# Kernel optimization log

Hardware: AMD Instinct MI355X
Metric: run time of the kernel (lower is better)

## Reference

```python
import jax, jax.numpy as jnp
import numpy as np
from jax import lax

B, G, D, S = 1, 2048, 64, 2
H_FULL = 200
H0 = H_FULL // 2 ** (S - 1)
PC_RANGE = (-50.0, -50.0, -4.0, 50.0, 50.0, 4.0)
THRESH = 0.05
CHUNK = 128


def conv3x3(x, w):
    # x: [b,c,h,w], w: [o,i,3,3]
    return lax.conv_general_dilated(x, w, (1, 1), 'SAME',
                                    dimension_numbers=('NCHW', 'OIHW', 'NCHW'))


def instance_norm(x, eps=1e-5):
    mu = x.mean(axis=(2, 3), keepdims=True)
    var = x.var(axis=(2, 3), keepdims=True)
    return (x - mu) / jnp.sqrt(var + eps)


def basic_block(x, w1, w2):
    # conv-(BN@init=identity)-relu-conv-(BN)-add-relu
    h = jax.nn.relu(conv3x3(x, w1))
    h = conv3x3(h, w2)
    return jax.nn.relu(x + h)


def upsampling_add(x, skip, w):
    b, c, h, wd = x.shape
    xu = jax.image.resize(x, (b, c, 2 * h, 2 * wd), method='bilinear')
    xu = instance_norm(conv3x3(xu, w))
    return xu + skip


def render_stage(means, cov6, feats, opac, mask, H, W):
    # Orthographic BEV splatting (3DGS-style EWA + front-to-back compositing).
    g, d = feats.shape
    sh = H / 100.0
    sw = W / 100.0
    # full_proj_transform: px = -sh*y + H/2 ; py = -sw*x + W/2
    u = -sh * means[:, 1] + 0.5 * H
    v = -sw * means[:, 0] + 0.5 * W
    # cov2d = J Sigma J^T + 0.3*I, J = [[0,-sh,0],[-sw,0,0]]
    a = sh * sh * cov6[:, 3] + 0.3
    c = sw * sw * cov6[:, 0] + 0.3
    bb = sh * sw * cov6[:, 1]
    det = jnp.maximum(a * c - bb * bb, 1e-8)
    A = c / det
    Bc = -bb / det
    C = a / det
    xs = jnp.arange(W, dtype=jnp.float32)
    ys = jnp.arange(H, dtype=jnp.float32)
    nc = g // CHUNK

    def step(carry, inp):
        T, out = carry
        u_, v_, A_, B_, C_, op_, mk_, ft_ = inp
        dx = u_[:, None, None] - xs[None, None, :]
        dy = v_[:, None, None] - ys[None, :, None]
        power = (-0.5 * (A_[:, None, None] * dx * dx + C_[:, None, None] * dy * dy)
                 - B_[:, None, None] * dx * dy)
        alpha = jnp.minimum(op_[:, None, None] * jnp.exp(power), 0.99)
        alpha = jnp.where((alpha >= 1.0 / 255.0) & mk_[:, None, None] & (power <= 0.0),
                          alpha, 0.0)
        cp = jnp.cumprod(1.0 - alpha, axis=0)
        t_exc = jnp.concatenate([jnp.ones_like(cp[:1]), cp[:-1]], 0) * T
        out = out + jnp.einsum('ghw,gd->dhw', alpha * t_exc, ft_)
        return (T * cp[-1], out), None

    ch = lambda arr: arr.reshape(nc, CHUNK, *arr.shape[1:])
    init = (jnp.ones((H, W), jnp.float32), jnp.zeros((d, H, W), jnp.float32))
    (_, out), _ = lax.scan(step, init,
                           (ch(u), ch(v), ch(A), ch(Bc), ch(C), ch(opac), ch(mask), ch(feats)))
    return out  # bg color = 0


def setup_inputs() -> dict:
    key = jax.random.key(0)
    ks = jax.random.split(key, 10)
    features = jax.random.normal(ks[0], (B, G, D), jnp.float32)
    xy = jax.random.uniform(ks[1], (B, G, 2), jnp.float32, -55.0, 55.0)
    z = jax.random.uniform(ks[2], (B, G, 1), jnp.float32, -5.0, 5.0)
    means3D = jnp.concatenate([xy, z], -1)
    L = jax.random.normal(ks[3], (B, G, 3, 3), jnp.float32) * 0.5
    Sig = jnp.einsum('bgij,bgkj->bgik', L, L) + 0.1 * jnp.eye(3, dtype=jnp.float32)
    cov3D = jnp.stack([Sig[..., 0, 0], Sig[..., 0, 1], Sig[..., 0, 2],
                       Sig[..., 1, 1], Sig[..., 1, 2], Sig[..., 2, 2]], -1)
    opacities = jax.random.uniform(ks[4], (B, G, S), jnp.float32)
    w_scale = 1.0 / np.sqrt(D * 9)
    bev_emb = jax.random.normal(ks[5], (H0 * H0, D), jnp.float32) * 0.02
    conv1_w = jax.random.normal(ks[6], (S, D, D, 3, 3), jnp.float32) * w_scale
    blk_w = jax.random.normal(ks[7], (S, 2, 2, D, D, 3, 3), jnp.float32) * w_scale
    up_w = jax.random.normal(ks[8], (S - 1, D, D, 3, 3), jnp.float32) * w_scale
    return {'features': features, 'means3D': means3D, 'cov3D': cov3D,
            'opacities': opacities, 'bev_emb': bev_emb, 'conv1_w': conv1_w,
            'blk_w': blk_w, 'up_w': up_w}


def reference(features, means3D, cov3D, opacities, bev_emb, conv1_w, blk_w, up_w):
    b = features.shape[0]
    d = features.shape[-1]
    m = means3D
    mask_pos = ((m[..., 0] >= PC_RANGE[0]) & (m[..., 0] <= PC_RANGE[3]) &
                (m[..., 1] >= PC_RANGE[1]) & (m[..., 1] <= PC_RANGE[4]) &
                (m[..., 2] >= PC_RANGE[2]) & (m[..., 2] <= PC_RANGE[5]))
    num_g = jnp.float32(0.0)
    bevs = []
    for s in range(S):
        H = H0 * 2 ** s
        mask = (opacities[..., s] > THRESH) & mask_pos
        rend = jax.vmap(lambda mn, cv, ft, op, mk: render_stage(mn, cv, ft, op, mk, H, H))
        bevs.append(rend(means3D, cov3D, features, opacities[..., s], mask))
        num_g = num_g + jnp.mean(jnp.sum(mask.astype(jnp.float32), 1))
    x = jnp.broadcast_to(jnp.transpose(bev_emb.reshape(H0, H0, d), (2, 0, 1))[None],
                         (b, d, H0, H0))
    for s in range(S):
        bev = conv3x3(bevs[s], conv1_w[s])
        if s == 0:
            x = x + bev
        else:
            x = upsampling_add(x, bev, up_w[s - 1])
        for blk in range(2):
            x = basic_block(x, blk_w[s, blk, 0], blk_w[s, blk, 1])
    return x, num_g
```

## Files before the change

### kernel.cpp

```cpp
#include <hip/hip_runtime.h>
#include <math.h>

#define G_N 2048
#define CCH 256
#define PSTR 12
#define NBLK 1024
#define WC (64 * 64 * 9)

typedef short bhalf8 __attribute__((ext_vector_type(8)));
typedef float f32x4 __attribute__((ext_vector_type(4)));
typedef unsigned short u16;

__device__ __forceinline__ u16 f2bf(float f) {
    unsigned u = __float_as_uint(f);
    unsigned r = (u + 0x7fffu + ((u >> 16) & 1u)) >> 16;
    return (u16)r;
}
__device__ __forceinline__ float b2f(u16 h) {
    return __uint_as_float((unsigned)h << 16);
}

__device__ __forceinline__ void chstore4(u16* p, ushort4 v) {
    union { unsigned long long u; ushort4 s; } x; x.s = v;
    __hip_atomic_store((unsigned long long*)p, x.u,
                       __ATOMIC_RELAXED, __HIP_MEMORY_SCOPE_AGENT);
}
__device__ __forceinline__ void cstore8(float* p, float a, float b) {
    union { unsigned long long u; float f[2]; } x;
    x.f[0] = a; x.f[1] = b;
    __hip_atomic_store((unsigned long long*)p, x.u,
                       __ATOMIC_RELAXED, __HIP_MEMORY_SCOPE_AGENT);
}
__device__ __forceinline__ float cload(const float* p) {
    return __hip_atomic_load(p, __ATOMIC_RELAXED, __HIP_MEMORY_SCOPE_AGENT);
}
__device__ __forceinline__ int iload(const int* p) {
    return __hip_atomic_load(p, __ATOMIC_RELAXED, __HIP_MEMORY_SCOPE_AGENT);
}

__device__ __forceinline__ void gbar(int* leaf, int* root, int* flag, int phase) {
    asm volatile("s_waitcnt vmcnt(0) lgkmcnt(0)" ::: "memory");
    __syncthreads();
    if (threadIdx.x == 0) {
        int g = blockIdx.x >> 5;
        int old = atomicAdd(&leaf[g * 16], 1);
        if ((old & 31) == 31) {
            int o2 = atomicAdd(root, 1);
            if ((o2 & 31) == 31)
                __hip_atomic_store(flag, phase, __ATOMIC_RELAXED,
                                   __HIP_MEMORY_SCOPE_AGENT);
        }
        while (__hip_atomic_load(flag, __ATOMIC_RELAXED,
                                 __HIP_MEMORY_SCOPE_AGENT) < phase)
            __builtin_amdgcn_s_sleep(16);
    }
    __syncthreads();
    asm volatile("" ::: "memory");
}

__device__ __forceinline__ void render_tile(
    int unit, const float* __restrict__ params,
    const float* __restrict__ feats, u16* __restrict__ out0,
    u16* __restrict__ out1, char* smem)
{
    int s = (unit < 169) ? 0 : 1;
    int t = (s == 0) ? unit : unit - 169;
    int tw = (s == 0) ? 13 : 25;
    int bxx = t % tw, byy = t / tw;
    int H = 100 << s;
    const float* P = params + s * G_N * PSTR;
    u16* out = s ? out1 : out0;

    float* raw = (float*)smem;
    float* cmp = raw + CCH * PSTR;
    int* s_wsum = (int*)(smem + 24576);

    int tid = threadIdx.x;
    int w = tid >> 6, lane = tid & 63;
    int x0 = bxx * 8, y0 = byy * 8;
    int px = x0 + (lane & 7), py = y0 + (lane >> 3);
    bool active = (px < H) && (py < H);
    float fx = (float)px, fy = (float)py;
    float tx0 = (float)x0, tx1 = (float)min(H - 1, x0 + 7);
    float ty0 = (float)y0, ty1 = (float)min(H - 1, y0 + 7);

    f32x4 acc[4];
#pragma unroll
    for (int k = 0; k < 4; ++k) acc[k] = (f32x4){0.f, 0.f, 0.f, 0.f};
    float T = 1.f;

    for (int base = 0; base < G_N; base += CCH) {
        int anyalive = __syncthreads_or((int)(active && T > 1e-6f));
        if (!anyalive) break;
        for (int i = tid; i < CCH * 3; i += 256)
            ((float4*)raw)[i] = ((const float4*)(P + base * PSTR))[i];
        __syncthreads();
        float u = raw[tid * PSTR + 0], v = raw[tid * PSTR + 1];
        float rx = raw[tid * PSTR + 8], ry = raw[tid * PSTR + 9];
        bool pass = (u + rx >= tx0) && (u - rx <= tx1) &&
                    (v + ry >= ty0) && (v - ry <= ty1);
        unsigned long long bal = __ballot(pass);
        int prefix = __popcll(bal & ((1ull << lane) - 1ull));
        if (lane == 0) s_wsum[w] = __popcll(bal);
        __syncthreads();
        int woff = 0;
        for (int k = 0; k < 4; ++k) if (k < w) woff += s_wsum[k];
        if (pass) {
            float4* dst = (float4*)(cmp + (woff + prefix) * PSTR);
            const float4* src = (const float4*)(raw + tid * PSTR);
            dst[0] = src[0]; dst[1] = src[1]; dst[2] = src[2];
        }
        __syncthreads();
        int nc = s_wsum[0] + s_wsum[1] + s_wsum[2] + s_wsum[3];
        if (active && T > 1e-6f) {
            for (int j = 0; j < nc; ++j) {
                float4 q0 = *(const float4*)(cmp + j * PSTR);
                float4 q1 = *(const float4*)(cmp + j * PSTR + 4);
                float dx = q0.x - fx, dy = q0.y - fy;
                float power = -0.5f * (q0.z * dx * dx + q1.x * dy * dy) - q0.w * dx * dy;
                if (power <= 0.f && power >= q1.z) {
                    float alpha = fminf(q1.y * __expf(power), 0.99f);
                    float wgt = alpha * T;
                    const f32x4* f4 = (const f32x4*)(feats + __float_as_int(q1.w) * 64) + w * 4;
#pragma unroll
                    for (int k = 0; k < 4; ++k) {
                        f32x4 fv = f4[k];
                        acc[k][0] = fmaf(wgt, fv[0], acc[k][0]);
                        acc[k][1] = fmaf(wgt, fv[1], acc[k][1]);
                        acc[k][2] = fmaf(wgt, fv[2], acc[k][2]);
                        acc[k][3] = fmaf(wgt, fv[3], acc[k][3]);
                    }
                    T *= (1.f - alpha);
                }
            }
        }
    }

    __syncthreads();
    float* shf = (float*)smem;
#pragma unroll
    for (int k = 0; k < 4; ++k)
        *(float4*)&shf[lane * 68 + w * 16 + k * 4] =
            (float4){acc[k][0], acc[k][1], acc[k][2], acc[k][3]};
    __syncthreads();
    for (int j = tid; j < 1024; j += 256) {
        int lp = j >> 4, c4 = (j & 15) * 4;
        int gy = y0 + (lp >> 3), gx = x0 + (lp & 7);
        if (gy < H && gx < H) {
            float4 v = *(float4*)&shf[lp * 68 + c4];
            ushort4 o = { f2bf(v.x), f2bf(v.y), f2bf(v.z), f2bf(v.w) };
            chstore4(&out[((gy * H + gx) << 6) + c4], o);
        }
    }
}

__device__ __forceinline__ void conv_tile(
    int bx, int H, const u16* __restrict__ in, const u16* __restrict__ wp,
    const float* __restrict__ bev, u16* __restrict__ outb,
    int ups, int dostats, float* __restrict__ sacc, char* smem)
{
    u16* xlds = (u16*)smem;
    u16* fin  = (u16*)(smem + 14400);
    float* red = (float*)(smem + 25600);

    int tid = threadIdx.x;
    int gw = (H + 7) >> 3;
    int by = bx / gw, bxx = bx - by * gw;
    int y0 = by * 8, x0 = bxx * 8;
    int w = tid >> 6, lane = tid & 63;
    int n = lane & 15, q = lane >> 4;
    int Hh = H >> 1;
    int oy = (y0 >> 1) - 2, ox = (x0 >> 1) - 2;

    if (ups) {
        for (int i = tid; i < 512; i += 256) {
            int px = i >> 3, c8 = (i & 7) * 8;
            int iy = px >> 3, ix = px & 7;
            int gyi = oy + iy, gxi = ox + ix;
            uint4 v = {0, 0, 0, 0};
            if (gyi >= 0 && gyi < Hh && gxi >= 0 && gxi < Hh)
                v = *(const uint4*)&in[((gyi * Hh + gxi) << 6) + c8];
            *(uint4*)&fin[px * 72 + c8] = v;
        }
        __syncthreads();
        for (int i = tid; i < 1600; i += 256) {
            int px = i >> 4, c4 = (i & 15) * 4;
            int yy = px / 10, xx = px - yy * 10;
            int gy = y0 - 1 + yy, gx = x0 - 1 + xx;
            ushort4 v = {0, 0, 0, 0};
            if (gy >= 0 && gy < H && gx >= 0 && gx < H) {
                int yi = gy >> 1, xi = gx >> 1;
                int yb = (gy & 1) ? min(yi + 1, Hh - 1) : max(yi - 1, 0);
                int xb = (gx & 1) ? min(xi + 1, Hh - 1) : max(xi - 1, 0);
                int t0 = yi - oy, t1 = xi - ox, t2 = yb - oy, t3 = xb - ox;
                ushort4 f00 = *(const ushort4*)&fin[(t0 * 8 + t1) * 72 + c4];
                ushort4 f01 = *(const ushort4*)&fin[(t0 * 8 + t3) * 72 + c4];
                ushort4 f10 = *(const ushort4*)&fin[(t2 * 8 + t1) * 72 + c4];
                ushort4 f11 = *(const ushort4*)&fin[(t2 * 8 + t3) * 72 + c4];
                v.x = f2bf(0.5625f * b2f(f00.x) + 0.1875f * (b2f(f01.x) + b2f(f10.x)) + 0.0625f * b2f(f11.x));
                v.y = f2bf(0.5625f * b2f(f00.y) + 0.1875f * (b2f(f01.y) + b2f(f10.y)) + 0.0625f * b2f(f11.y));
                v.z = f2bf(0.5625f * b2f(f00.z) + 0.1875f * (b2f(f01.z) + b2f(f10.z)) + 0.0625f * b2f(f11.z));
                v.w = f2bf(0.5625f * b2f(f00.w) + 0.1875f * (b2f(f01.w) + b2f(f10.w)) + 0.0625f * b2f(f11.w));
            }
            *(ushort4*)&xlds[px * 72 + c4] = v;
        }
    } else {
        for (int i = tid; i < 800; i += 256) {
            int px = i >> 3, c8 = (i & 7) * 8;
            int yy = px / 10, xx = px - yy * 10;
            int gy = y0 - 1 + yy, gx = x0 - 1 + xx;
            uint4 v = {0, 0, 0, 0};
            if (gy >= 0 && gy < H && gx >= 0 && gx < H)
                v = *(const uint4*)&in[((gy * H + gx) << 6) + c8];
            *(uint4*)&xlds[px * 72 + c8] = v;
        }
    }
    __syncthreads();

    f32x4 acc[4];
#pragma unroll
    for (int m = 0; m < 4; ++m) acc[m] = (f32x4){0.f, 0.f, 0.f, 0.f};
    const bhalf8* wp8 = (const bhalf8*)wp;
    int sy = 2 * w + (n >> 3), sx = n & 7;

    bhalf8 a0 = wp8[0 * 64 + lane];
    bhalf8 a1 = wp8[1 * 64 + lane];
    bhalf8 a2 = wp8[2 * 64 + lane];
    bhalf8 a3 = wp8[3 * 64 + lane];
    bhalf8 bb = *(const bhalf8*)&xlds[(sy * 10 + sx) * 72 + q * 8];

#pragma unroll 1
    for (int p = 0; p < 18; ++p) {
        bhalf8 na0, na1, na2, na3, nbb;
        if (p < 17) {
            int pn = p + 1;
            na0 = wp8[(pn * 4 + 0) * 64 + lane];
            na1 = wp8[(pn * 4 + 1) * 64 + lane];
            na2 = wp8[(pn * 4 + 2) * 64 + lane];
            na3 = wp8[(pn * 4 + 3) * 64 + lane];
            int tap = pn >> 1, ch = pn & 1;
            int dy = tap / 3, dx = tap - dy * 3;
            nbb = *(const bhalf8*)&xlds[((sy + dy) * 10 + sx + dx) * 72 + ch * 32 + q * 8];
        }
        acc[0] = __builtin_amdgcn_mfma_f32_16x16x32_bf16(a0, bb, acc[0], 0, 0, 0);
        acc[1] = __builtin_amdgcn_mfma_f32_16x16x32_bf16(a1, bb, acc[1], 0, 0, 0);
        acc[2] = __builtin_amdgcn_mfma_f32_16x16x32_bf16(a2, bb, acc[2], 0, 0, 0);
        acc[3] = __builtin_amdgcn_mfma_f32_16x16x32_bf16(a3, bb, acc[3], 0, 0, 0);
        a0 = na0; a1 = na1; a2 = na2; a3 = na3; bb = nbb;
    }

    int gy = y0 + sy, gx = x0 + sx;
    if (gy < H && gx < H) {
        int base = (gy * H + gx) << 6;
#pragma unroll
        for (int m = 0; m < 4; ++m) {
            int oc0 = m * 16 + q * 4;
            float v0 = acc[m][0], v1 = acc[m][1], v2 = acc[m][2], v3 = acc[m][3];
            if (bev) {
                float4 av = *(const float4*)&bev[base + oc0];
                v0 += av.x; v1 += av.y; v2 += av.z; v3 += av.w;
            }
            ushort4 o = { f2bf(v0), f2bf(v1), f2bf(v2), f2bf(v3) };
            chstore4(&outb[base + oc0], o);
        }
    }

    if (dostats) {
#pragma unroll
        for (int m = 0; m < 4; ++m)
#pragma unroll
            for (int r = 0; r < 4; ++r) {
                float v = acc[m][r];
                float s = v, s2 = v * v;
#pragma unroll
                for (int d = 1; d < 16; d <<= 1) {
                    s += __shfl_xor(s, d, 64);
                    s2 += __shfl_xor(s2, d, 64);
                }
                if (n == 0) {
                    int oc = m * 16 + q * 4 + r;
                    red[w * 128 + oc] = s;
                    red[w * 128 + 64 + oc] = s2;
                }
            }
        __syncthreads();
        if (tid < 128) {
            float t = red[tid] + red[128 + tid] + red[256 + tid] + red[384 + tid];
            atomicAdd(&sacc[tid], t);
        }
    }
}

__device__ __forceinline__ void bb_tile(
    int bx, int H, const u16* __restrict__ in,
    const u16* __restrict__ wp1, const u16* __restrict__ wp2,
    u16* __restrict__ outb, float* __restrict__ outf, int final_,
    int nrm, const u16* __restrict__ nskip, const float* __restrict__ sraw,
    char* smem)
{
    u16* xin  = (u16*)smem;
    u16* ilds = (u16*)(smem + 20736);
    float* nm = (float*)(smem + 35136);
    float* nr = nm + 64;

    int tid = threadIdx.x;
    int gw = (H + 7) >> 3;
    int by = bx / gw, bxx = bx - by * gw;
    int y0 = by * 8, x0 = bxx * 8;
    int w = tid >> 6, lane = tid & 63;
    int n = lane & 15, q = lane >> 4;

    if (nrm) {
        if (tid < 64) {
            float s = cload(&sraw[tid]), s2 = cload(&sraw[64 + tid]);
            float mean = s * (1.f / 40000.f);
            float var = s2 * (1.f / 40000.f) - mean * mean;
            nm[tid] = mean;
            nr[tid] = rsqrtf(var + 1e-5f);
        }
        __syncthreads();
        for (int i = tid; i < 2304; i += 256) {
            int px = i >> 4, c4 = (i & 15) * 4;
            int yy = px / 12, xx = px - yy * 12;
            int gy = y0 - 2 + yy, gx = x0 - 2 + xx;
            ushort4 v = {0, 0, 0, 0};
            if (gy >= 0 && gy < H && gx >= 0 && gx < H) {
                int off = ((gy * H + gx) << 6) + c4;
                ushort4 a = *(const ushort4*)&in[off];
                ushort4 b = *(const ushort4*)&nskip[off];
                v.x = f2bf((b2f(a.x) - nm[c4 + 0]) * nr[c4 + 0] + b2f(b.x));
                v.y = f2bf((b2f(a.y) - nm[c4 + 1]) * nr[c4 + 1] + b2f(b.y));
                v.z = f2bf((b2f(a.z) - nm[c4 + 2]) * nr[c4 + 2] + b2f(b.z));
                v.w = f2bf((b2f(a.w) - nm[c4 + 3]) * nr[c4 + 3] + b2f(b.w));
            }
            *(ushort4*)&xin[px * 72 + c4] = v;
        }
    } else {
        for (int i = tid; i < 1152; i += 256) {
            int px = i >> 3, c8 = (i & 7) * 8;
            int yy = px / 12, xx = px - yy * 12;
            int gy = y0 - 2 + yy, gx = x0 - 2 + xx;
            uint4 v = {0, 0, 0, 0};
            if (gy >= 0 && gy < H && gx >= 0 && gx < H)
                v = *(const uint4*)&in[((gy * H + gx) << 6) + c8];
            *(uint4*)&xin[px * 72 + c8] = v;
        }
    }
    __syncthreads();

    const bhalf8* w1 = (const bhalf8*)wp1;
#pragma unroll 1
    for (int r = 0; r < 2; ++r) {
        int t = w + 4 * r;
        int px = t * 16 + n;
        bool val = px < 100;
        int pc = val ? px : 0;
        int yy = pc / 10, xx = pc - yy * 10;

        f32x4 acc[4];
#pragma unroll
        for (int m = 0; m < 4; ++m) acc[m] = (f32x4){0.f, 0.f, 0.f, 0.f};

        bhalf8 a0 = w1[0 * 64 + lane];
        bhalf8 a1 = w1[1 * 64 + lane];
        bhalf8 a2 = w1[2 * 64 + lane];
        bhalf8 a3 = w1[3 * 64 + lane];
        bhalf8 bb = *(const bhalf8*)&xin[(yy * 12 + xx) * 72 + q * 8];

#pragma unroll 1
        for (int p = 0; p < 18; ++p) {
            bhalf8 na0, na1, na2, na3, nbb;
            if (p < 17) {
                int pn = p + 1;
                na0 = w1[(pn * 4 + 0) * 64 + lane];
                na1 = w1[(pn * 4 + 1) * 64 + lane];
                na2 = w1[(pn * 4 + 2) * 64 + lane];
                na3 = w1[(pn * 4 + 3) * 64 + lane];
                int tap = pn >> 1, ch = pn & 1;
                int dy = tap / 3, dx = tap - dy * 3;
                nbb = *(const bhalf8*)&xin[((yy + dy) * 12 + xx + dx) * 72 + ch * 32 + q * 8];
            }
            acc[0] = __builtin_amdgcn_mfma_f32_16x16x32_bf16(a0, bb, acc[0], 0, 0, 0);
            acc[1] = __builtin_amdgcn_mfma_f32_16x16x32_bf16(a1, bb, acc[1], 0, 0, 0);
            acc[2] = __builtin_amdgcn_mfma_f32_16x16x32_bf16(a2, bb, acc[2], 0, 0, 0);
            acc[3] = __builtin_amdgcn_mfma_f32_16x16x32_bf16(a3, bb, acc[3], 0, 0, 0);
            a0 = na0; a1 = na1; a2 = na2; a3 = na3; bb = nbb;
        }

        int iy = y0 - 1 + yy, ix = x0 - 1 + xx;
        bool ok = val && iy >= 0 && iy < H && ix >= 0 && ix < H;
        if (val) {
#pragma unroll
            for (int m = 0; m < 4; ++m) {
                ushort4 o = {0, 0, 0, 0};
                if (ok) {
                    o.x = f2bf(fmaxf(acc[m][0], 0.f));
                    o.y = f2bf(fmaxf(acc[m][1], 0.f));
                    o.z = f2bf(fmaxf(acc[m][2], 0.f));
                    o.w = f2bf(fmaxf(acc[m][3], 0.f));
                }
                *(ushort4*)&ilds[px * 72 + m * 16 + q * 4] = o;
            }
        }
    }
    __syncthreads();

    f32x4 acc[4];
#pragma unroll
    for (int m = 0; m < 4; ++m) acc[m] = (f32x4){0.f, 0.f, 0.f, 0.f};
    const bhalf8* w2 = (const bhalf8*)wp2;
    int sy = 2 * w + (n >> 3), sx = n & 7;

    bhalf8 a0 = w2[0 * 64 + lane];
    bhalf8 a1 = w2[1 * 64 + lane];
    bhalf8 a2 = w2[2 * 64 + lane];
    bhalf8 a3 = w2[3 * 64 + lane];
    bhalf8 bb = *(const bhalf8*)&ilds[(sy * 10 + sx) * 72 + q * 8];

#pragma unroll 1
    for (int p = 0; p < 18; ++p) {
        bhalf8 na0, na1, na2, na3, nbb;
        if (p < 17) {
            int pn = p + 1;
            na0 = w2[(pn * 4 + 0) * 64 + lane];
            na1 = w2[(pn * 4 + 1) * 64 + lane];
            na2 = w2[(pn * 4 + 2) * 64 + lane];
            na3 = w2[(pn * 4 + 3) * 64 + lane];
            int tap = pn >> 1, ch = pn & 1;
            int dy = tap / 3, dx = tap - dy * 3;
            nbb = *(const bhalf8*)&ilds[((sy + dy) * 10 + sx + dx) * 72 + ch * 32 + q * 8];
        }
        acc[0] = __builtin_amdgcn_mfma_f32_16x16x32_bf16(a0, bb, acc[0], 0, 0, 0);
        acc[1] = __builtin_amdgcn_mfma_f32_16x16x32_bf16(a1, bb, acc[1], 0, 0, 0);
        acc[2] = __builtin_amdgcn_mfma_f32_16x16x32_bf16(a2, bb, acc[2], 0, 0, 0);
        acc[3] = __builtin_amdgcn_mfma_f32_16x16x32_bf16(a3, bb, acc[3], 0, 0, 0);
        a0 = na0; a1 = na1; a2 = na2; a3 = na3; bb = nbb;
    }

    int gy = y0 + sy, gx = x0 + sx;
    if (gy < H && gx < H) {
        int base = (gy * H + gx) << 6;
#pragma unroll
        for (int m = 0; m < 4; ++m) {
            int oc0 = m * 16 + q * 4;
            ushort4 xr = *(const ushort4*)&xin[((sy + 2) * 12 + sx + 2) * 72 + oc0];
            float v0 = fmaxf(acc[m][0] + b2f(xr.x), 0.f);
            float v1 = fmaxf(acc[m][1] + b2f(xr.y), 0.f);
            float v2 = fmaxf(acc[m][2] + b2f(xr.z), 0.f);
            float v3 = fmaxf(acc[m][3] + b2f(xr.w), 0.f);
            if (final_) {
                int pix = gy * H + gx;
                outf[(oc0 + 0) * H * H + pix] = v0;
                outf[(oc0 + 1) * H * H + pix] = v1;
                outf[(oc0 + 2) * H * H + pix] = v2;
                outf[(oc0 + 3) * H * H + pix] = v3;
            } else {
                ushort4 o = { f2bf(v0), f2bf(v1), f2bf(v2), f2bf(v3) };
                chstore4(&outb[base + oc0], o);
            }
        }
    }
}

__global__ __launch_bounds__(256, 4) void gls_mega(
    const float* __restrict__ feats, const float* __restrict__ bev_emb,
    const float* __restrict__ conv1_w, const float* __restrict__ blk_w,
    const float* __restrict__ up_w, const float* __restrict__ means,
    const float* __restrict__ cov6, const float* __restrict__ opac,
    u16* __restrict__ wprep, float* __restrict__ params, int* __restrict__ cnts,
    u16* __restrict__ R0h, u16* __restrict__ X0h,
    u16* __restrict__ X1h, u16* __restrict__ X2h,
    u16* __restrict__ Qr0h, u16* __restrict__ Sh,
    u16* __restrict__ Uh, u16* __restrict__ Y1h,
    float* __restrict__ out, int* __restrict__ barmem, float* __restrict__ sacc)
{
    __shared__ __align__(16) char smem[36352];
    int bid = blockIdx.x;
    int tid = threadIdx.x;
    int* leaf = barmem;
    int* root = barmem + 512;
    int* flag = barmem + 513;
    int ph = 0;

    if (bid < 16) {
        int item = bid * 256 + tid;
        int s = item >> 11, g = item & 2047;
        float mx = means[g * 3 + 0], my = means[g * 3 + 1], mz = means[g * 3 + 2];
        float op = opac[g * 2 + s];
        bool mask = (mx >= -50.f && mx <= 50.f && my >= -50.f && my <= 50.f &&
                     mz >= -4.f && mz <= 4.f && op > 0.05f);
        float Hs = (float)(100 << s), sh = (float)(1 << s);
        float u = 0.f, v = 0.f, A = 0.f, B = 0.f, C = 0.f, pthr = 0.f;
        float rx = -1.f, ry = -1.f;
        if (mask) {
            u = -sh * my + 0.5f * Hs;
            v = -sh * mx + 0.5f * Hs;
            float a = sh * sh * cov6[g * 6 + 3] + 0.3f;
            float c = sh * sh * cov6[g * 6 + 0] + 0.3f;
            float bb = sh * sh * cov6[g * 6 + 1];
            float det = fmaxf(a * c - bb * bb, 1e-8f);
            float t = logf(255.f * op);
            A = c / det; B = -bb / det; C = a / det;
            pthr = -t;
            rx = sqrtf(2.f * t * a); ry = sqrtf(2.f * t * c);
        }
        float* Q = params + (s * G_N + g) * PSTR;
        cstore8(&Q[0], u, v);
        cstore8(&Q[2], A, B);
        cstore8(&Q[4], C, op);
        cstore8(&Q[6], pthr, __int_as_float(g));
        cstore8(&Q[8], rx, ry);
        unsigned long long bal = __ballot(mask);
        if ((tid & 63) == 0) atomicAdd(&cnts[s], __popcll(bal));
    }
    gbar(leaf, root, flag, ++ph);

    if (bid < 794) {
        render_tile(bid, params, feats, R0h, Qr0h, smem);
    } else if (bid < 992) {
        int rb = bid - 794;
        int p = rb % 18, c = rb / 18;
        const float* src;
        if (c == 0) src = conv1_w;
        else if (c <= 4) src = blk_w + (c - 1) * WC;
        else if (c == 5) src = conv1_w + WC;
        else if (c == 6) src = up_w;
        else src = blk_w + (c - 3) * WC;
        int tap = p >> 1;
        int m = tid >> 6, lane = tid & 63;
        int oc = m * 16 + (lane & 15);
        int ci0 = (p & 1) * 32 + (lane >> 4) * 8;
        u16 v[8];
#pragma unroll
        for (int j = 0; j < 8; ++j)
            v[j] = f2bf(src[(oc * 64 + ci0 + j) * 9 + tap]);
        u16* dst = wprep + ((c * 18 + p) * 4 + m) * 64 * 8 + lane * 8;
        chstore4(dst, (ushort4){v[0], v[1], v[2], v[3]});
        chstore4(dst + 4, (ushort4){v[4], v[5], v[6], v[7]});
    }
    gbar(leaf, root, flag, ++ph);

    if (bid < 169)
        conv_tile(bid, 100, R0h, wprep + 0 * WC, bev_emb, X0h, 0, 0, nullptr, smem);
    gbar(leaf, root, flag, ++ph);

    if (bid < 169)
        bb_tile(bid, 100, X0h, wprep + 1 * WC, wprep + 2 * WC, X1h,
                nullptr, 0, 0, nullptr, nullptr, smem);
    else if (bid < 481)
        conv_tile(bid - 169, 200, Qr0h, wprep + 5 * WC, nullptr, Sh, 0, 0, nullptr, smem);
    gbar(leaf, root, flag, ++ph);

    if (bid < 169)
        bb_tile(bid, 100, X1h, wprep + 3 * WC, wprep + 4 * WC, X2h,
                nullptr, 0, 0, nullptr, nullptr, smem);
    else if (bid < 482)
        conv_tile(312 + bid - 169, 200, Qr0h, wprep + 5 * WC, nullptr, Sh, 0, 0, nullptr, smem);
    gbar(leaf, root, flag, ++ph);

    if (bid < 625)
        conv_tile(bid, 200, X2h, wprep + 6 * WC, nullptr, Uh, 1, 1, sacc, smem);
    gbar(leaf, root, flag, ++ph);

    if (bid < 625)
        bb_tile(bid, 200, Uh, wprep + 7 * WC, wprep + 8 * WC, Y1h,
                nullptr, 0, 1, Sh, sacc, smem);
    gbar(leaf, root, flag, ++ph);

    if (bid == 0 && threadIdx.x == 0)
        out[2560000] = (float)(iload(&cnts[0]) + iload(&cnts[1]));
    if (bid < 625)
        bb_tile(bid, 200, Y1h, wprep + 9 * WC, wprep + 10 * WC, nullptr,
                out, 1, 0, nullptr, nullptr, smem);
}

extern "C" void kernel_launch(void* const* d_in, const int* in_sizes, int n_in,
                              void* d_out, int out_size, void* d_ws, size_t ws_size,
                              hipStream_t stream)
{
    const float* feats   = (const float*)d_in[0];
    const float* means   = (const float*)d_in[1];
    const float* cov6    = (const float*)d_in[2];
    const float* opac    = (const float*)d_in[3];
    const float* bev_emb = (const float*)d_in[4];
    const float* conv1_w = (const float*)d_in[5];
    const float* blk_w   = (const float*)d_in[6];
    const float* up_w    = (const float*)d_in[7];
    float* out = (float*)d_out;
    float* ws = (float*)d_ws;

    float* P      = ws;
    int*   cnts   = (int*)(ws + 49152);
    int*   barmem = (int*)(ws + 49280);
    float* sacc   = ws + 49856;
    u16*   wprep  = (u16*)(ws + 50176);

    u16* R0h  = (u16*)(ws + 262144);
    u16* X0h  = (u16*)(ws + 589824);
    u16* X1h  = (u16*)(ws + 917504);
    u16* X2h  = (u16*)(ws + 1245184);
    u16* Qr0h = (u16*)(ws + 1572864);
    u16* Sh   = (u16*)(ws + 2883584);
    u16* Uh   = (u16*)(ws + 4194304);
    u16* Y1h  = (u16*)(ws + 5505024);

    hipMemsetAsync(cnts, 0, (49984 - 49152) * 4, stream);
    gls_mega<<<NBLK, 256, 0, stream>>>(feats, bev_emb, conv1_w, blk_w, up_w,
                                       means, cov6, opac, wprep, P, cnts,
                                       R0h, X0h, X1h, X2h, Qr0h, Sh, Uh, Y1h,
                                       out, barmem, sacc);
    (void)in_sizes; (void)n_in; (void)out_size; (void)ws_size;
}
```

Baseline: 260.0 us.

## Triple-buffer MFMA operand prefetch and stage conv outputs through LDS for wide stores

Replaces the single-step software pipeline in the conv and basic-block MFMA loops with a fully unrolled loop that prefetches weights and LDS activations three steps ahead. This is meant to hide global/LDS load latency behind the MFMA chain. Conv and render epilogues now gather each tile's output in LDS and write 16-byte-per-thread contiguous stores instead of scattered 8-byte ones, at the cost of extra __syncthreads and higher register pressure under the 4-waves-per-SIMD launch bound.

```diff
diff --git a/kernel.cpp b/kernel.cpp
--- a/kernel.cpp
+++ b/kernel.cpp
@@ -20,16 +20,21 @@
     return __uint_as_float((unsigned)h << 16);
 }
 
-__device__ __forceinline__ void chstore4(u16* p, ushort4 v) {
-    union { unsigned long long u; ushort4 s; } x; x.s = v;
-    __hip_atomic_store((unsigned long long*)p, x.u,
+__device__ __forceinline__ void chstore8u(void* p, unsigned long long u) {
+    __hip_atomic_store((unsigned long long*)p, u,
                        __ATOMIC_RELAXED, __HIP_MEMORY_SCOPE_AGENT);
+}
+__device__ __forceinline__ void chstore16(void* p, uint4 v) {
+    union { uint2 d; unsigned long long u; } a, b;
+    a.d = (uint2){v.x, v.y};
+    b.d = (uint2){v.z, v.w};
+    chstore8u(p, a.u);
+    chstore8u((char*)p + 8, b.u);
 }
 __device__ __forceinline__ void cstore8(float* p, float a, float b) {
     union { unsigned long long u; float f[2]; } x;
     x.f[0] = a; x.f[1] = b;
-    __hip_atomic_store((unsigned long long*)p, x.u,
-                       __ATOMIC_RELAXED, __HIP_MEMORY_SCOPE_AGENT);
+    chstore8u(p, x.u);
 }
 __device__ __forceinline__ float cload(const float* p) {
     return __hip_atomic_load(p, __ATOMIC_RELAXED, __HIP_MEMORY_SCOPE_AGENT);
@@ -57,6 +62,40 @@
     __syncthreads();
     asm volatile("" ::: "memory");
 }
+
+#define KLOOP3(WPTR, LDSPTR, SY, SX, ACC)                                      \
+    {                                                                          \
+        const bhalf8* wp8_ = (const bhalf8*)(WPTR);                            \
+        bhalf8 A0_[3], A1_[3], A2_[3], A3_[3], Bv_[3];                         \
+        _Pragma("unroll")                                                      \
+        for (int i_ = 0; i_ < 3; ++i_) {                                       \
+            A0_[i_] = wp8_[(i_ * 4 + 0) * 64 + lane];                          \
+            A1_[i_] = wp8_[(i_ * 4 + 1) * 64 + lane];                          \
+            A2_[i_] = wp8_[(i_ * 4 + 2) * 64 + lane];                          \
+            A3_[i_] = wp8_[(i_ * 4 + 3) * 64 + lane];                          \
+            int tap_ = i_ >> 1, ch_ = i_ & 1;                                  \
+            int dy_ = tap_ / 3, dx_ = tap_ - dy_ * 3;                          \
+            Bv_[i_] = *(const bhalf8*)&(LDSPTR)[(((SY) + dy_) * 10 + (SX) + dx_) * 72 + ch_ * 32 + q * 8]; \
+        }                                                                      \
+        _Pragma("unroll")                                                      \
+        for (int p_ = 0; p_ < 18; ++p_) {                                      \
+            int sl_ = p_ % 3;                                                  \
+            ACC[0] = __builtin_amdgcn_mfma_f32_16x16x32_bf16(A0_[sl_], Bv_[sl_], ACC[0], 0, 0, 0); \
+            ACC[1] = __builtin_amdgcn_mfma_f32_16x16x32_bf16(A1_[sl_], Bv_[sl_], ACC[1], 0, 0, 0); \
+            ACC[2] = __builtin_amdgcn_mfma_f32_16x16x32_bf16(A2_[sl_], Bv_[sl_], ACC[2], 0, 0, 0); \
+            ACC[3] = __builtin_amdgcn_mfma_f32_16x16x32_bf16(A3_[sl_], Bv_[sl_], ACC[3], 0, 0, 0); \
+            int pn_ = p_ + 3;                                                  \
+            if (pn_ < 18) {                                                    \
+                A0_[sl_] = wp8_[(pn_ * 4 + 0) * 64 + lane];                    \
+                A1_[sl_] = wp8_[(pn_ * 4 + 1) * 64 + lane];                    \
+                A2_[sl_] = wp8_[(pn_ * 4 + 2) * 64 + lane];                    \
+                A3_[sl_] = wp8_[(pn_ * 4 + 3) * 64 + lane];                    \
+                int tap_ = pn_ >> 1, ch_ = pn_ & 1;                            \
+                int dy_ = tap_ / 3, dx_ = tap_ - dy_ * 3;                      \
+                Bv_[sl_] = *(const bhalf8*)&(LDSPTR)[(((SY) + dy_) * 10 + (SX) + dx_) * 72 + ch_ * 32 + q * 8]; \
+            }                                                                  \
+        }                                                                      \
+    }
 
 __device__ __forceinline__ void render_tile(
     int unit, const float* __restrict__ params,
@@ -143,13 +182,18 @@
         *(float4*)&shf[lane * 68 + w * 16 + k * 4] =
             (float4){acc[k][0], acc[k][1], acc[k][2], acc[k][3]};
     __syncthreads();
-    for (int j = tid; j < 1024; j += 256) {
-        int lp = j >> 4, c4 = (j & 15) * 4;
+    for (int j = tid; j < 512; j += 256) {
+        int lp = j >> 3, c8 = (j & 7) * 8;
         int gy = y0 + (lp >> 3), gx = x0 + (lp & 7);
         if (gy < H && gx < H) {
-            float4 v = *(float4*)&shf[lp * 68 + c4];
-            ushort4 o = { f2bf(v.x), f2bf(v.y), f2bf(v.z), f2bf(v.w) };
-            chstore4(&out[((gy * H + gx) << 6) + c4], o);
+            float4 va = *(float4*)&shf[lp * 68 + c8];
+            float4 vb = *(float4*)&shf[lp * 68 + c8 + 4];
+            union { u16 s[8]; uint4 u; } pk;
+            pk.s[0] = f2bf(va.x); pk.s[1] = f2bf(va.y);
+            pk.s[2] = f2bf(va.z); pk.s[3] = f2bf(va.w);
+            pk.s[4] = f2bf(vb.x); pk.s[5] = f2bf(vb.y);
+            pk.s[6] = f2bf(vb.z); pk.s[7] = f2bf(vb.w);
+            chstore16(&out[((gy * H + gx) << 6) + c8], pk.u);
         }
     }
 }
@@ -220,48 +264,35 @@
     f32x4 acc[4];
 #pragma unroll
     for (int m = 0; m < 4; ++m) acc[m] = (f32x4){0.f, 0.f, 0.f, 0.f};
-    const bhalf8* wp8 = (const bhalf8*)wp;
     int sy = 2 * w + (n >> 3), sx = n & 7;
-
-    bhalf8 a0 = wp8[0 * 64 + lane];
-    bhalf8 a1 = wp8[1 * 64 + lane];
-    bhalf8 a2 = wp8[2 * 64 + lane];
-    bhalf8 a3 = wp8[3 * 64 + lane];
-    bhalf8 bb = *(const bhalf8*)&xlds[(sy * 10 + sx) * 72 + q * 8];
-
-#pragma unroll 1
-    for (int p = 0; p < 18; ++p) {
-        bhalf8 na0, na1, na2, na3, nbb;
-        if (p < 17) {
-            int pn = p + 1;
-            na0 = wp8[(pn * 4 + 0) * 64 + lane];
-            na1 = wp8[(pn * 4 + 1) * 64 + lane];
-            na2 = wp8[(pn * 4 + 2) * 64 + lane];
-            na3 = wp8[(pn * 4 + 3) * 64 + lane];
-            int tap = pn >> 1, ch = pn & 1;
-            int dy = tap / 3, dx = tap - dy * 3;
-            nbb = *(const bhalf8*)&xlds[((sy + dy) * 10 + sx + dx) * 72 + ch * 32 + q * 8];
-        }
-        acc[0] = __builtin_amdgcn_mfma_f32_16x16x32_bf16(a0, bb, acc[0], 0, 0, 0);
-        acc[1] = __builtin_amdgcn_mfma_f32_16x16x32_bf16(a1, bb, acc[1], 0, 0, 0);
-        acc[2] = __builtin_amdgcn_mfma_f32_16x16x32_bf16(a2, bb, acc[2], 0, 0, 0);
-        acc[3] = __builtin_amdgcn_mfma_f32_16x16x32_bf16(a3, bb, acc[3], 0, 0, 0);
-        a0 = na0; a1 = na1; a2 = na2; a3 = na3; bb = nbb;
-    }
+    KLOOP3(wp, xlds, sy, sx, acc);
 
     int gy = y0 + sy, gx = x0 + sx;
-    if (gy < H && gx < H) {
-        int base = (gy * H + gx) << 6;
-#pragma unroll
-        for (int m = 0; m < 4; ++m) {
-            int oc0 = m * 16 + q * 4;
-            float v0 = acc[m][0], v1 = acc[m][1], v2 = acc[m][2], v3 = acc[m][3];
-            if (bev) {
-                float4 av = *(const float4*)&bev[base + oc0];
-                v0 += av.x; v1 += av.y; v2 += av.z; v3 += av.w;
-            }
-            ushort4 o = { f2bf(v0), f2bf(v1), f2bf(v2), f2bf(v3) };
-            chstore4(&outb[base + oc0], o);
+    bool ok = (gy < H) && (gx < H);
+    int base = ok ? ((gy * H + gx) << 6) : 0;
+    ushort4 ov[4];
+#pragma unroll
+    for (int m = 0; m < 4; ++m) {
+        int oc0 = m * 16 + q * 4;
+        float v0 = acc[m][0], v1 = acc[m][1], v2 = acc[m][2], v3 = acc[m][3];
+        if (bev && ok) {
+            float4 av = *(const float4*)&bev[base + oc0];
+            v0 += av.x; v1 += av.y; v2 += av.z; v3 += av.w;
+        }
+        ov[m] = (ushort4){ f2bf(v0), f2bf(v1), f2bf(v2), f2bf(v3) };
+    }
+    __syncthreads();
+    int lp = sy * 8 + sx;
+#pragma unroll
+    for (int m = 0; m < 4; ++m)
+        *(ushort4*)&xlds[lp * 72 + m * 16 + q * 4] = ov[m];
+    __syncthreads();
+    for (int j = tid; j < 512; j += 256) {
+        int pp = j >> 3, c8 = (j & 7) * 8;
+        int gy2 = y0 + (pp >> 3), gx2 = x0 + (pp & 7);
+        if (gy2 < H && gx2 < H) {
+            uint4 v = *(uint4*)&xlds[pp * 72 + c8];
+            chstore16(&outb[((gy2 * H + gx2) << 6) + c8], v);
         }
     }
 
@@ -348,7 +379,6 @@
     }
     __syncthreads();
 
-    const bhalf8* w1 = (const bhalf8*)wp1;
 #pragma unroll 1
     for (int r = 0; r < 2; ++r) {
         int t = w + 4 * r;
@@ -357,47 +387,54 @@
         int pc = val ? px : 0;
         int yy = pc / 10, xx = pc - yy * 10;
 
-        f32x4 acc[4];
-#pragma unroll
-        for (int m = 0; m < 4; ++m) acc[m] = (f32x4){0.f, 0.f, 0.f, 0.f};
-
-        bhalf8 a0 = w1[0 * 64 + lane];
-        bhalf8 a1 = w1[1 * 64 + lane];
-        bhalf8 a2 = w1[2 * 64 + lane];
-        bhalf8 a3 = w1[3 * 64 + lane];
-        bhalf8 bb = *(const bhalf8*)&xin[(yy * 12 + xx) * 72 + q * 8];
-
-#pragma unroll 1
-        for (int p = 0; p < 18; ++p) {
-            bhalf8 na0, na1, na2, na3, nbb;
-            if (p < 17) {
-                int pn = p + 1;
-                na0 = w1[(pn * 4 + 0) * 64 + lane];
-                na1 = w1[(pn * 4 + 1) * 64 + lane];
-                na2 = w1[(pn * 4 + 2) * 64 + lane];
-                na3 = w1[(pn * 4 + 3) * 64 + lane];
-                int tap = pn >> 1, ch = pn & 1;
-                int dy = tap / 3, dx = tap - dy * 3;
-                nbb = *(const bhalf8*)&xin[((yy + dy) * 12 + xx + dx) * 72 + ch * 32 + q * 8];
-            }
-            acc[0] = __builtin_amdgcn_mfma_f32_16x16x32_bf16(a0, bb, acc[0], 0, 0, 0);
-            acc[1] = __builtin_amdgcn_mfma_f32_16x16x32_bf16(a1, bb, acc[1], 0, 0, 0);
-            acc[2] = __builtin_amdgcn_mfma_f32_16x16x32_bf16(a2, bb, acc[2], 0, 0, 0);
-            acc[3] = __builtin_amdgcn_mfma_f32_16x16x32_bf16(a3, bb, acc[3], 0, 0, 0);
-            a0 = na0; a1 = na1; a2 = na2; a3 = na3; bb = nbb;
+        f32x4 acc1[4];
+#pragma unroll
+        for (int m = 0; m < 4; ++m) acc1[m] = (f32x4){0.f, 0.f, 0.f, 0.f};
+
+        {
+            const bhalf8* wp8_ = (const bhalf8*)wp1;
+            bhalf8 A0_[3], A1_[3], A2_[3], A3_[3], Bv_[3];
+#pragma unroll
+            for (int i_ = 0; i_ < 3; ++i_) {
+                A0_[i_] = wp8_[(i_ * 4 + 0) * 64 + lane];
+                A1_[i_] = wp8_[(i_ * 4 + 1) * 64 + lane];
+                A2_[i_] = wp8_[(i_ * 4 + 2) * 64 + lane];
+                A3_[i_] = wp8_[(i_ * 4 + 3) * 64 + lane];
+                int tap_ = i_ >> 1, ch_ = i_ & 1;
+                int dy_ = tap_ / 3, dx_ = tap_ - dy_ * 3;
+                Bv_[i_] = *(const bhalf8*)&xin[((yy + dy_) * 12 + xx + dx_) * 72 + ch_ * 32 + q * 8];
+            }
+#pragma unroll
+            for (int p_ = 0; p_ < 18; ++p_) {
+                int sl_ = p_ % 3;
+                acc1[0] = __builtin_amdgcn_mfma_f32_16x16x32_bf16(A0_[sl_], Bv_[sl_], acc1[0], 0, 0, 0);
+                acc1[1] = __builtin_amdgcn_mfma_f32_16x16x32_bf16(A1_[sl_], Bv_[sl_], acc1[1], 0, 0, 0);
+                acc1[2] = __builtin_amdgcn_mfma_f32_16x16x32_bf16(A2_[sl_], Bv_[sl_], acc1[2], 0, 0, 0);
+                acc1[3] = __builtin_amdgcn_mfma_f32_16x16x32_bf16(A3_[sl_], Bv_[sl_], acc1[3], 0, 0, 0);
+                int pn_ = p_ + 3;
+                if (pn_ < 18) {
+                    A0_[sl_] = wp8_[(pn_ * 4 + 0) * 64 + lane];
+                    A1_[sl_] = wp8_[(pn_ * 4 + 1) * 64 + lane];
+                    A2_[sl_] = wp8_[(pn_ * 4 + 2) * 64 + lane];
+                    A3_[sl_] = wp8_[(pn_ * 4 + 3) * 64 + lane];
+                    int tap_ = pn_ >> 1, ch_ = pn_ & 1;
+                    int dy_ = tap_ / 3, dx_ = tap_ - dy_ * 3;
+                    Bv_[sl_] = *(const bhalf8*)&xin[((yy + dy_) * 12 + xx + dx_) * 72 + ch_ * 32 + q * 8];
+                }
+            }
         }
 
         int iy = y0 - 1 + yy, ix = x0 - 1 + xx;
-        bool ok = val && iy >= 0 && iy < H && ix >= 0 && ix < H;
+        bool ok1 = val && iy >= 0 && iy < H && ix >= 0 && ix < H;
         if (val) {
 #pragma unroll
             for (int m = 0; m < 4; ++m) {
                 ushort4 o = {0, 0, 0, 0};
-                if (ok) {
-                    o.x = f2bf(fmaxf(acc[m][0], 0.f));
-                    o.y = f2bf(fmaxf(acc[m][1], 0.f));
-                    o.z = f2bf(fmaxf(acc[m][2], 0.f));
-                    o.w = f2bf(fmaxf(acc[m][3], 0.f));
+                if (ok1) {
+                    o.x = f2bf(fmaxf(acc1[m][0], 0.f));
+                    o.y = f2bf(fmaxf(acc1[m][1], 0.f));
+                    o.z = f2bf(fmaxf(acc1[m][2], 0.f));
+                    o.w = f2bf(fmaxf(acc1[m][3], 0.f));
                 }
                 *(ushort4*)&ilds[px * 72 + m * 16 + q * 4] = o;
             }
@@ -408,55 +445,49 @@
     f32x4 acc[4];
 #pragma unroll
     for (int m = 0; m < 4; ++m) acc[m] = (f32x4){0.f, 0.f, 0.f, 0.f};
-    const bhalf8* w2 = (const bhalf8*)wp2;
     int sy = 2 * w + (n >> 3), sx = n & 7;
-
-    bhalf8 a0 = w2[0 * 64 + lane];
-    bhalf8 a1 = w2[1 * 64 + lane];
-    bhalf8 a2 = w2[2 * 64 + lane];
-    bhalf8 a3 = w2[3 * 64 + lane];
-    bhalf8 bb = *(const bhalf8*)&ilds[(sy * 10 + sx) * 72 + q * 8];
-
-#pragma unroll 1
-    for (int p = 0; p < 18; ++p) {
-        bhalf8 na0, na1, na2, na3, nbb;
-        if (p < 17) {
-            int pn = p + 1;
-            na0 = w2[(pn * 4 + 0) * 64 + lane];
-            na1 = w2[(pn * 4 + 1) * 64 + lane];
-            na2 = w2[(pn * 4 + 2) * 64 + lane];
-            na3 = w2[(pn * 4 + 3) * 64 + lane];
-            int tap = pn >> 1, ch = pn & 1;
-            int dy = tap / 3, dx = tap - dy * 3;
-            nbb = *(const bhalf8*)&ilds[((sy + dy) * 10 + sx + dx) * 72 + ch * 32 + q * 8];
-        }
-        acc[0] = __builtin_amdgcn_mfma_f32_16x16x32_bf16(a0, bb, acc[0], 0, 0, 0);
-        acc[1] = __builtin_amdgcn_mfma_f32_16x16x32_bf16(a1, bb, acc[1], 0, 0, 0);
-        acc[2] = __builtin_amdgcn_mfma_f32_16x16x32_bf16(a2, bb, acc[2], 0, 0, 0);
-        acc[3] = __builtin_amdgcn_mfma_f32_16x16x32_bf16(a3, bb, acc[3], 0, 0, 0);
-        a0 = na0; a1 = na1; a2 = na2; a3 = na3; bb = nbb;
-    }
+    KLOOP3(wp2, ilds, sy, sx, acc);
 
     int gy = y0 + sy, gx = x0 + sx;
-    if (gy < H && gx < H) {
-        int base = (gy * H + gx) << 6;
-#pragma unroll
-        for (int m = 0; m < 4; ++m) {
-            int oc0 = m * 16 + q * 4;
-            ushort4 xr = *(const ushort4*)&xin[((sy + 2) * 12 + sx + 2) * 72 + oc0];
-            float v0 = fmaxf(acc[m][0] + b2f(xr.x), 0.f);
-            float v1 = fmaxf(acc[m][1] + b2f(xr.y), 0.f);
-            float v2 = fmaxf(acc[m][2] + b2f(xr.z), 0.f);
-            float v3 = fmaxf(acc[m][3] + b2f(xr.w), 0.f);
-            if (final_) {
-                int pix = gy * H + gx;
-                outf[(oc0 + 0) * H * H + pix] = v0;
-                outf[(oc0 + 1) * H * H + pix] = v1;
-                outf[(oc0 + 2) * H * H + pix] = v2;
-                outf[(oc0 + 3) * H * H + pix] = v3;
-            } else {
-                ushort4 o = { f2bf(v0), f2bf(v1), f2bf(v2), f2bf(v3) };
-                chstore4(&outb[base + oc0], o);
+    bool ok = (gy < H) && (gx < H);
+    ushort4 ov[4];
+    float vf[4][4];
+#pragma unroll
+    for (int m = 0; m < 4; ++m) {
+        int oc0 = m * 16 + q * 4;
+        ushort4 xr = *(const ushort4*)&xin[((sy + 2) * 12 + sx + 2) * 72 + oc0];
+        vf[m][0] = fmaxf(acc[m][0] + b2f(xr.x), 0.f);
+        vf[m][1] = fmaxf(acc[m][1] + b2f(xr.y), 0.f);
+        vf[m][2] = fmaxf(acc[m][2] + b2f(xr.z), 0.f);
+        vf[m][3] = fmaxf(acc[m][3] + b2f(xr.w), 0.f);
+        ov[m] = (ushort4){ f2bf(vf[m][0]), f2bf(vf[m][1]), f2bf(vf[m][2]), f2bf(vf[m][3]) };
+    }
+
+    if (final_) {
+        if (ok) {
+            int pix = gy * H + gx;
+#pragma unroll
+            for (int m = 0; m < 4; ++m) {
+                int oc0 = m * 16 + q * 4;
+                outf[(oc0 + 0) * H * H + pix] = vf[m][0];
+                outf[(oc0 + 1) * H * H + pix] = vf[m][1];
+                outf[(oc0 + 2) * H * H + pix] = vf[m][2];
+                outf[(oc0 + 3) * H * H + pix] = vf[m][3];
+            }
+        }
+    } else {
+        __syncthreads();
+        int lp = sy * 8 + sx;
+#pragma unroll
+        for (int m = 0; m < 4; ++m)
+            *(ushort4*)&xin[lp * 72 + m * 16 + q * 4] = ov[m];
+        __syncthreads();
+        for (int j = tid; j < 512; j += 256) {
+            int pp = j >> 3, c8 = (j & 7) * 8;
+            int gy2 = y0 + (pp >> 3), gx2 = x0 + (pp & 7);
+            if (gy2 < H && gx2 < H) {
+                uint4 v = *(uint4*)&xin[pp * 72 + c8];
+                chstore16(&outb[((gy2 * H + gx2) << 6) + c8], v);
             }
         }
     }
@@ -530,13 +561,12 @@
         int m = tid >> 6, lane = tid & 63;
         int oc = m * 16 + (lane & 15);
         int ci0 = (p & 1) * 32 + (lane >> 4) * 8;
-        u16 v[8];
+        union { u16 s[8]; uint4 u; } pk;
 #pragma unroll
         for (int j = 0; j < 8; ++j)
-            v[j] = f2bf(src[(oc * 64 + ci0 + j) * 9 + tap]);
+            pk.s[j] = f2bf(src[(oc * 64 + ci0 + j) * 9 + tap]);
         u16* dst = wprep + ((c * 18 + p) * 4 + m) * 64 * 8 + lane * 8;
-        chstore4(dst, (ushort4){v[0], v[1], v[2], v[3]});
-        chstore4(dst + 4, (ushort4){v[4], v[5], v[6], v[7]});
+        chstore16(dst, pk.u);
     }
     gbar(leaf, root, flag, ++ph);
 
```

Measured after the change: 430.7 us. 65.7% more time.
